# Kernel tuning notes

Measured on AMD Instinct MI355X. Metric: run time of the kernel, lower is better.

## Reference

```python
import jax, jax.numpy as jnp
import numpy as np

B, N, D = 32, 20, 64          # graph pairs, max node set size, node state dim
NODE_F, EDGE_F = 16, 8        # raw feature dims
E_PER, PROP = 40, 5           # edges per graph, propagation steps
NC2 = N * (N - 1) // 2        # 190
TEMP, ITERS = 0.1, 20         # sinkhorn temperature / iterations
SRC, DST = np.triu_indices(N, 1)   # source_list / destination_list (len NC2)


def _lin(k, fin, fout):
    return jax.random.normal(k, (fin, fout), dtype=jnp.float32) / np.sqrt(fin).astype(np.float32)


def setup_inputs():
    key = jax.random.key(0)
    ks = jax.random.split(key, 24)
    tn, te = 2 * B * N, 2 * B * E_PER
    gid = jnp.repeat(jnp.arange(2 * B), E_PER)   # edges stay within their graph
    inp = {
        'node_features': jax.random.normal(ks[0], (tn, NODE_F), jnp.float32),
        'edge_features': jax.random.normal(ks[1], (te, EDGE_F), jnp.float32),
        'query_adj': (jax.random.uniform(ks[2], (B, N, N)) < 0.3).astype(jnp.float32),
        'corpus_adj': (jax.random.uniform(ks[3], (B, N, N)) < 0.3).astype(jnp.float32),
        'from_idx': jax.random.randint(ks[4], (te,), 0, N) + gid * N,
        'to_idx': jax.random.randint(ks[5], (te,), 0, N) + gid * N,
    }
    # GraphEncoder
    inp['Wn'] = _lin(ks[6], NODE_F, D); inp['bn'] = jnp.zeros(D)
    inp['We'] = _lin(ks[7], EDGE_F, D); inp['be'] = jnp.zeros(D)
    # GraphPropLayer: message net (in 3D) and node-update net (in 2D)
    inp['Wm1'] = _lin(ks[8], 3 * D, D); inp['bm1'] = jnp.zeros(D)
    inp['Wm2'] = _lin(ks[9], D, D);     inp['bm2'] = jnp.zeros(D)
    inp['Wu1'] = _lin(ks[10], 2 * D, D); inp['bu1'] = jnp.zeros(D)
    inp['Wu2'] = _lin(ks[11], D, D);     inp['bu2'] = jnp.zeros(D)
    # node_sinkhorn_feature_layers: Linear(D,N) -> ReLU -> Linear(N,N)
    inp['Ws1'] = _lin(ks[12], D, N); inp['bs1'] = jnp.zeros(N)
    inp['Ws2'] = _lin(ks[13], N, N); inp['bs2'] = jnp.zeros(N)
    # lrl_network: Linear(2D+1, D) -> ReLU -> Linear(D, D)
    inp['Wl1'] = _lin(ks[14], 2 * D + 1, D); inp['bl1'] = jnp.zeros(D)
    inp['Wl2'] = _lin(ks[15], D, D);         inp['bl2'] = jnp.zeros(D)
    return inp


def _mlp2(x, W1, b1, W2, b2):
    return jax.nn.relu(x @ W1 + b1) @ W2 + b2


def _sinkhorn(log_alpha):
    la = log_alpha / TEMP
    for _ in range(ITERS):
        la = la - jax.nn.logsumexp(la, axis=2, keepdims=True)
        la = la - jax.nn.logsumexp(la, axis=1, keepdims=True)
    return jnp.exp(la)


def _nc2_edge_emb(H, adj, Wl1, bl1, Wl2, bl2):
    s, d = H[:, SRC], H[:, DST]          # [B, NC2, D]
    e = adj[:, SRC, DST][..., None]      # [B, NC2, 1]
    fwd = _mlp2(jnp.concatenate([s, d, e], -1), Wl1, bl1, Wl2, bl2)
    bwd = _mlp2(jnp.concatenate([d, s, e], -1), Wl1, bl1, Wl2, bl2)
    return fwd + bwd


def reference(node_features, edge_features, query_adj, corpus_adj, from_idx, to_idx,
              Wn, bn, We, be, Wm1, bm1, Wm2, bm2, Wu1, bu1, Wu2, bu2,
              Ws1, bs1, Ws2, bs2, Wl1, bl1, Wl2, bl2):
    # encoder
    h = node_features @ Wn + bn
    e = edge_features @ We + be
    # GMN-style gather -> MLP -> scatter propagation
    for _ in range(PROP):
        msg = _mlp2(jnp.concatenate([h[from_idx], h[to_idx], e], -1), Wm1, bm1, Wm2, bm2)
        agg = jax.ops.segment_sum(msg, to_idx, num_segments=2 * B * N)
        h = _mlp2(jnp.concatenate([h, agg], -1), Wu1, bu1, Wu2, bu2)
    # split_and_stack (all graphs have exactly N nodes): query even, corpus odd
    H = h.reshape(2 * B, N, D)
    Hq, Hc = H[0::2], H[1::2]
    # node Sinkhorn over L1 cdist of transformed features
    Tq = _mlp2(Hq, Ws1, bs1, Ws2, bs2)
    Tc = _mlp2(Hc, Ws1, bs1, Ws2, bs2)
    cost = jnp.abs(Tq[:, :, None, :] - Tc[:, None, :, :]).sum(-1)   # [B, N, N]
    P = _sinkhorn(-cost)                                            # node transport plan
    qe = _nc2_edge_emb(Hq, query_adj, Wl1, bl1, Wl2, bl2)           # [B, NC2, D]
    ce = _nc2_edge_emb(Hc, corpus_adj, Wl1, bl1, Wl2, bl2)
    # 4-way gather-multiply edge scores: [B, NC2, NC2]
    straight = P[:, SRC[:, None], SRC[None, :]] * P[:, DST[:, None], DST[None, :]]
    cross = P[:, SRC[:, None], DST[None, :]] * P[:, DST[:, None], SRC[None, :]]
    esi = jnp.maximum(straight, cross)                              # use_max=True
    eplan = _sinkhorn(jnp.log(esi + 1e-6))                          # use_second_sinkhorn_log
    # use_m_ms_edge=True: pairwise asymmetric L1 alignment distance
    diff = qe[:, :, None, :] - ce[:, None, :, :]                    # [B, NC2, NC2, D]
    dist = (eplan * (jax.nn.relu(diff).sum(-1) + jax.nn.relu(-diff).sum(-1))).sum((-1, -2))
    return dist                                                      # [B]
```

## Files before the change

kernel.cpp:

```cpp
#include <hip/hip_runtime.h>
#include <math.h>

#define B_     32
#define N_     20
#define D_     64
#define NODE_F 16
#define EDGE_F 8
#define E_PER  40
#define PROP   5
#define NC2    190
#define ITERS  20
#define INV_TEMP 10.0f
#define TN (2*B_*N_)
#define NG (2*B_)

struct PairTab { int s[NC2]; int d[NC2]; };
constexpr PairTab make_pairs() {
    PairTab t{};
    int idx = 0;
    for (int i = 0; i < N_; ++i)
        for (int j = i + 1; j < N_; ++j) { t.s[idx] = i; t.d[idx] = j; ++idx; }
    return t;
}
__device__ constexpr PairTab PAIRS = make_pairs();

__device__ __forceinline__ float rlane(float x, int k) {
    return __int_as_float(__builtin_amdgcn_readlane(__float_as_int(x), k));
}
template<int CTRL>
__device__ __forceinline__ float dppmov(float x) {
    return __int_as_float(__builtin_amdgcn_update_dpp(
        0, __float_as_int(x), CTRL, 0xf, 0xf, false));
}
__device__ __forceinline__ float rowsum16(float x) {
    x += dppmov<0x121>(x); x += dppmov<0x122>(x);
    x += dppmov<0x124>(x); x += dppmov<0x128>(x);
    return x;
}
__device__ __forceinline__ float rowmax16(float x) {
    x = fmaxf(x, dppmov<0x121>(x)); x = fmaxf(x, dppmov<0x122>(x));
    x = fmaxf(x, dppmov<0x124>(x)); x = fmaxf(x, dppmov<0x128>(x));
    return x;
}
__device__ __forceinline__ float nrcp(float x) {
    float r = __builtin_amdgcn_rcpf(x);
    r = r * fmaf(-x, r, 2.0f);
    return r;
}

__global__ __launch_bounds__(640) void k_prop(
    const float* __restrict__ nf, const float* __restrict__ ef,
    const int* __restrict__ fidx, const int* __restrict__ tidx,
    const float* __restrict__ Wn, const float* __restrict__ bn,
    const float* __restrict__ We, const float* __restrict__ be,
    const float* __restrict__ Wm1, const float* __restrict__ bm1,
    const float* __restrict__ Wm2, const float* __restrict__ bm2,
    const float* __restrict__ Wu1, const float* __restrict__ bu1,
    const float* __restrict__ Wu2, const float* __restrict__ bu2,
    float* __restrict__ hout)
{
    __shared__ float sh[20][64];
    __shared__ float se[40][64];
    __shared__ float sa[20][64];
    __shared__ short sF[40], sD[40];
    int g = blockIdx.x, t = threadIdx.x, w = t >> 6, l = t & 63;

    if (t < 40) {
        sF[t] = (short)(fidx[g * 40 + t] - g * 20);
        sD[t] = (short)(tidx[g * 40 + t] - g * 20);
    }
#pragma unroll
    for (int s = 0; s < 2; ++s) {
        int n = 2 * w + s;
        float a = bn[l];
#pragma unroll
        for (int k = 0; k < NODE_F; ++k) a += nf[(g * 20 + n) * NODE_F + k] * Wn[k * 64 + l];
        sh[n][l] = a; sa[n][l] = 0.f;
    }
#pragma unroll
    for (int s = 0; s < 4; ++s) {
        int e = 4 * w + s;
        float a = be[l];
#pragma unroll
        for (int k = 0; k < EDGE_F; ++k) a += ef[(g * 40 + e) * EDGE_F + k] * We[k * 64 + l];
        se[e][l] = a;
    }
    __syncthreads();

    for (int step = 0; step < PROP; ++step) {
        float xf[4], xt[4], xe[4]; int dst[4];
#pragma unroll
        for (int s = 0; s < 4; ++s) {
            int e = 4 * w + s;
            int fr = sF[e]; dst[s] = sD[e];
            xf[s] = sh[fr][l]; xt[s] = sh[dst[s]][l]; xe[s] = se[e][l];
        }
        float b1 = bm1[l];
        float acc[4];
#pragma unroll
        for (int s = 0; s < 4; ++s) acc[s] = b1;
#pragma unroll 4
        for (int k = 0; k < 64; ++k) {
            float w0 = Wm1[k * 64 + l];
            float w1 = Wm1[(64 + k) * 64 + l];
            float w2 = Wm1[(128 + k) * 64 + l];
#pragma unroll
            for (int s = 0; s < 4; ++s)
                acc[s] += rlane(xf[s], k) * w0 + rlane(xt[s], k) * w1 + rlane(xe[s], k) * w2;
        }
        float b2 = bm2[l];
        float out[4];
#pragma unroll
        for (int s = 0; s < 4; ++s) { acc[s] = fmaxf(acc[s], 0.f); out[s] = b2; }
#pragma unroll 4
        for (int k = 0; k < 64; ++k) {
            float ww = Wm2[k * 64 + l];
#pragma unroll
            for (int s = 0; s < 4; ++s) out[s] += rlane(acc[s], k) * ww;
        }
#pragma unroll
        for (int s = 0; s < 4; ++s) atomicAdd(&sa[dst[s]][l], out[s]);
        __syncthreads();

        float xh[2], xa[2];
#pragma unroll
        for (int s = 0; s < 2; ++s) {
            int n = 2 * w + s;
            xh[s] = sh[n][l]; xa[s] = sa[n][l];
        }
        float c1 = bu1[l];
        float a2[2];
#pragma unroll
        for (int s = 0; s < 2; ++s) a2[s] = c1;
#pragma unroll 4
        for (int k = 0; k < 64; ++k) {
            float wa = Wu1[k * 64 + l];
            float wb = Wu1[(64 + k) * 64 + l];
#pragma unroll
            for (int s = 0; s < 2; ++s)
                a2[s] += rlane(xh[s], k) * wa + rlane(xa[s], k) * wb;
        }
        float c2 = bu2[l];
        float o2[2];
#pragma unroll
        for (int s = 0; s < 2; ++s) { a2[s] = fmaxf(a2[s], 0.f); o2[s] = c2; }
#pragma unroll 4
        for (int k = 0; k < 64; ++k) {
            float ww = Wu2[k * 64 + l];
#pragma unroll
            for (int s = 0; s < 2; ++s) o2[s] += rlane(a2[s], k) * ww;
        }
#pragma unroll
        for (int s = 0; s < 2; ++s) {
            int n = 2 * w + s;
            sh[n][l] = o2[s]; sa[n][l] = 0.f;
        }
        __syncthreads();
    }
#pragma unroll
    for (int s = 0; s < 2; ++s) {
        int n = 2 * w + s;
        hout[(g * 20 + n) * 64 + l] = sh[n][l];
    }
}

__global__ __launch_bounds__(1024, 4) void k_fuse(
    const float* __restrict__ h,
    const float* __restrict__ qadj, const float* __restrict__ cadj,
    const float* __restrict__ Ws1, const float* __restrict__ bs1,
    const float* __restrict__ Ws2, const float* __restrict__ bs2,
    const float* __restrict__ Wl1, const float* __restrict__ bl1,
    const float* __restrict__ Wl2, const float* __restrict__ bl2,
    float* __restrict__ emb, float* __restrict__ eplan, float* __restrict__ dout)
{
    __shared__ short sQs[192], sQd[192];
    __shared__ float sP[N_][N_];
    __shared__ float sVbuf[192];
    __shared__ float region[12800];
    int t = threadIdx.x, w = t >> 6, l = t & 63;

    if (t < 192) {
        int tt = t < NC2 ? t : NC2 - 1;
        sQs[t] = (short)PAIRS.s[tt]; sQd[t] = (short)PAIRS.d[tt];
    }
    __syncthreads();

    if (blockIdx.x < 32) {
        int b = blockIdx.x;
        if (t == 0) dout[b] = 0.f;
        float* sT = region;
        float* sLa = region + 800;

        {
            int lk = (l < 20) ? l : 0;
#pragma unroll
            for (int s = 0; s < 3; ++s) {
                int r = w + 16 * s;
                if (r < 40) {
                    float hv = h[(b * 40 + r) * 64 + l];
                    float a = bs1[lk];
#pragma unroll 4
                    for (int ff = 0; ff < 64; ++ff) a += rlane(hv, ff) * Ws1[ff * 20 + lk];
                    a = fmaxf(a, 0.f);
                    float t2 = bs2[lk];
#pragma unroll
                    for (int j = 0; j < 20; ++j) t2 += rlane(a, j) * Ws2[j * 20 + lk];
                    if (l < 20) sT[(r >= 20) * 400 + (r % 20) * 20 + l] = t2;
                }
            }
        }
        __syncthreads();
        if (t < 400) {
            int i = t / 20, j = t % 20;
            float c = 0.f;
#pragma unroll
            for (int k = 0; k < 20; ++k) c += fabsf(sT[i * 20 + k] - sT[400 + j * 20 + k]);
            sLa[i * 20 + j] = -c * INV_TEMP;
        }
        __syncthreads();

        if (w == 0) {
            int q = l & 31, r2 = l >> 5;
            bool qok = (q < 20);
            float A20[10], u10[10];
#pragma unroll
            for (int i = 0; i < 10; ++i) {
                int r = 2 * i + r2;
                A20[i] = qok ? sLa[r * 20 + q] : -1e30f;
            }
            float vq = 0.f;
            for (int it = 0; it < ITERS; ++it) {
#pragma unroll
                for (int i = 0; i < 10; ++i) {
                    float x = A20[i] - vq;
                    float m = x;
#pragma unroll
                    for (int off = 16; off; off >>= 1) m = fmaxf(m, __shfl_xor(m, off));
                    float s = __expf(x - m);
#pragma unroll
                    for (int off = 16; off; off >>= 1) s += __shfl_xor(s, off);
                    u10[i] = m + __logf(s);
                }
                float pm = -1e30f;
#pragma unroll
                for (int i = 0; i < 10; ++i) pm = fmaxf(pm, A20[i] - u10[i]);
                float ps = 0.f;
#pragma unroll
                for (int i = 0; i < 10; ++i) ps += __expf(A20[i] - u10[i] - pm);
                float om = __shfl_xor(pm, 32), os = __shfl_xor(ps, 32);
                float M = fmaxf(pm, om);
                float S = ps * __expf(pm - M) + os * __expf(om - M);
                vq = M + __logf(S);
                if (!qok) vq = 0.f;
            }
#pragma unroll
            for (int i = 0; i < 10; ++i) {
                int r = 2 * i + r2;
                if (qok) sP[r][q] = __expf(A20[i] - u10[i] - vq);
            }
        }
        __syncthreads();

        int g4 = l >> 4, l16 = l & 15, rslot = w * 4 + g4;
        int sp[3], dp[3]; bool pv[3];
#pragma unroll
        for (int i = 0; i < 3; ++i) {
            int p = rslot + 64 * i;
            pv[i] = (p < NC2);
            int pc = pv[i] ? p : 0;
            sp[i] = sQs[pc]; dp[i] = sQd[pc];
        }
        int sq[12], dq[12]; bool qv[12];
#pragma unroll
        for (int j = 0; j < 12; ++j) {
            int q = l16 + 16 * j;
            qv[j] = (q < NC2);
            int qc = qv[j] ? q : 0;
            sq[j] = sQs[qc]; dq[j] = sQd[qc];
        }

        float AE[3][12];
#pragma unroll
        for (int i = 0; i < 3; ++i)
#pragma unroll
            for (int j = 0; j < 12; ++j) {
                if (pv[i] && qv[j]) {
                    float st = sP[sp[i]][sq[j]] * sP[dp[i]][dq[j]];
                    float cr = sP[sp[i]][dq[j]] * sP[dp[i]][sq[j]];
                    AE[i][j] = __logf(fmaxf(st, cr) + 1e-6f) * INV_TEMP;
                } else AE[i][j] = -1e30f;
            }

        float u[3];
#pragma unroll
        for (int i = 0; i < 3; ++i) {
            float m = -1e30f;
#pragma unroll
            for (int j = 0; j < 12; ++j) m = fmaxf(m, AE[i][j]);
            m = rowmax16(m);
            float s = 0.f;
#pragma unroll
            for (int j = 0; j < 12; ++j) s += __expf(AE[i][j] - m);
            s = rowsum16(s);
            u[i] = m + __logf(s);
            if (!pv[i]) u[i] = 0.f;
        }
#pragma unroll
        for (int j = 0; j < 12; ++j) {
            float pm = -1e30f;
#pragma unroll
            for (int i = 0; i < 3; ++i) if (pv[i]) pm = fmaxf(pm, AE[i][j] - u[i]);
            region[rslot * 200 + l16 + 16 * j] = pm;
        }
        __syncthreads();
        if (t < 192) {
            float M = -1e30f;
#pragma unroll
            for (int s = 0; s < 64; ++s) M = fmaxf(M, region[s * 200 + t]);
            sVbuf[t] = M;
        }
        __syncthreads();
        float Mj[12];
#pragma unroll
        for (int j = 0; j < 12; ++j) Mj[j] = sVbuf[l16 + 16 * j];
#pragma unroll
        for (int j = 0; j < 12; ++j) {
            float ps = 0.f;
#pragma unroll
            for (int i = 0; i < 3; ++i) if (pv[i]) ps += __expf(AE[i][j] - u[i] - Mj[j]);
            region[rslot * 200 + l16 + 16 * j] = ps;
        }
        __syncthreads();
        if (t < 192) {
            float S = 0.f;
#pragma unroll
            for (int s = 0; s < 64; ++s) S += region[s * 200 + t];
            sVbuf[t] = sVbuf[t] + __logf(fmaxf(S, 1e-37f));
        }
        __syncthreads();
#pragma unroll
        for (int j = 0; j < 12; ++j) Mj[j] = sVbuf[l16 + 16 * j];
#pragma unroll
        for (int i = 0; i < 3; ++i)
#pragma unroll
            for (int j = 0; j < 12; ++j) {
                float e = __expf(AE[i][j] - u[i] - Mj[j]);
                AE[i][j] = (pv[i] && qv[j]) ? e : 0.f;
            }
        __syncthreads();

        float invS[3];
        for (int it = 0; it < ITERS - 1; ++it) {
#pragma unroll
            for (int i = 0; i < 3; ++i) {
                float s01 = AE[i][0] + AE[i][1], s23 = AE[i][2] + AE[i][3];
                float s45 = AE[i][4] + AE[i][5], s67 = AE[i][6] + AE[i][7];
                float s89 = AE[i][8] + AE[i][9], sab = AE[i][10] + AE[i][11];
                float S = ((s01 + s23) + (s45 + s67)) + (s89 + sab);
                S = rowsum16(S);
                invS[i] = nrcp(fmaxf(S, 1e-30f));
            }
#pragma unroll
            for (int j = 0; j < 12; ++j) {
                float pc = AE[0][j] * invS[0];
                pc = fmaf(AE[1][j], invS[1], pc);
                pc = fmaf(AE[2][j], invS[2], pc);
                region[rslot * 200 + l16 + 16 * j] = pc;
            }
            __syncthreads();
            if (t < 192) {
                float a0 = 0.f, a1 = 0.f, a2 = 0.f, a3 = 0.f;
#pragma unroll
                for (int s = 0; s < 16; ++s) {
                    a0 += region[(4 * s + 0) * 200 + t];
                    a1 += region[(4 * s + 1) * 200 + t];
                    a2 += region[(4 * s + 2) * 200 + t];
                    a3 += region[(4 * s + 3) * 200 + t];
                }
                float c = (a0 + a1) + (a2 + a3);
                sVbuf[t] = nrcp(fmaxf(c, 1e-30f));
            }
            __syncthreads();
            float ic[12];
#pragma unroll
            for (int j = 0; j < 12; ++j) ic[j] = sVbuf[l16 + 16 * j];
#pragma unroll
            for (int i = 0; i < 3; ++i)
#pragma unroll
                for (int j = 0; j < 12; ++j) {
                    float tmp = AE[i][j] * invS[i];
                    AE[i][j] = tmp * ic[j];
                }
        }

        float* ep = eplan + (size_t)b * NC2 * NC2;
#pragma unroll
        for (int i = 0; i < 3; ++i) {
            if (pv[i]) {
                int p = rslot + 64 * i;
                float* row = ep + (size_t)p * NC2;
#pragma unroll
                for (int j = 0; j < 12; ++j)
                    if (qv[j]) row[l16 + 16 * j] = AE[i][j];
            }
        }
    } else {
        int eb = blockIdx.x - 32, b = eb >> 2, qt = eb & 3;
        float b1 = bl1[l];
        float w128 = Wl1[128 * 64 + l];
        float b2 = 2.f * bl2[l];

        int base = qt * 96 + w * 6;
        float sv[6], dv[6], av[6]; bool val[6]; int gg[6], pp[6];
#pragma unroll
        for (int s = 0; s < 6; ++s) {
            int pl = base + s;
            val[s] = (pl < 380);
            int plc = val[s] ? pl : 0;
            gg[s] = (plc >= 190) ? 1 : 0;
            pp[s] = plc - gg[s] * 190;
            int sp = sQs[pp[s]], dp = sQd[pp[s]];
            sv[s] = h[(b * 40 + gg[s] * 20 + sp) * 64 + l];
            dv[s] = h[(b * 40 + gg[s] * 20 + dp) * 64 + l];
            const float* adj = gg[s] ? cadj : qadj;
            av[s] = adj[b * 400 + sp * 20 + dp];
        }
        float aF[6], aB[6];
#pragma unroll
        for (int s = 0; s < 6; ++s) { float t0 = b1 + av[s] * w128; aF[s] = t0; aB[s] = t0; }
#pragma unroll 2
        for (int k = 0; k < 64; ++k) {
            float w0 = Wl1[k * 64 + l];
            float w1 = Wl1[(64 + k) * 64 + l];
#pragma unroll
            for (int s = 0; s < 6; ++s) {
                float a = rlane(sv[s], k), c = rlane(dv[s], k);
                aF[s] += a * w0 + c * w1;
                aB[s] += c * w0 + a * w1;
            }
        }
        float hs[6], out[6];
#pragma unroll
        for (int s = 0; s < 6; ++s) { hs[s] = fmaxf(aF[s], 0.f) + fmaxf(aB[s], 0.f); out[s] = b2; }
#pragma unroll 4
        for (int k = 0; k < 64; ++k) {
            float ww = Wl2[k * 64 + l];
#pragma unroll
            for (int s = 0; s < 6; ++s) out[s] += rlane(hs[s], k) * ww;
        }
#pragma unroll
        for (int s = 0; s < 6; ++s)
            if (val[s]) emb[((size_t)(2 * b + gg[s]) * NC2 + pp[s]) * 64 + l] = out[s];
    }
}

__global__ __launch_bounds__(256) void k_dist(
    const float* __restrict__ emb, const float* __restrict__ eplan, float* __restrict__ dout)
{
    int b = blockIdx.x, c = blockIdx.y;
    int w = threadIdx.x >> 6, l = threadIdx.x & 63;
    const float* qe = emb + (size_t)(2 * b) * NC2 * D_;
    const float* ce = emb + (size_t)(2 * b + 1) * NC2 * D_;
    const float* W = eplan + (size_t)b * NC2 * NC2;
    float acc = 0.f;
    int pbase = c * 16 + w * 4;
    for (int i = 0; i < 4; ++i) {
        int p = pbase + i;
        if (p >= NC2) break;
        float qv = qe[(size_t)p * D_ + l];
        const float* wrow = W + (size_t)p * NC2;
        for (int q = 0; q < NC2; ++q)
            acc += wrow[q] * fabsf(qv - ce[(size_t)q * D_ + l]);
    }
#pragma unroll
    for (int off = 32; off; off >>= 1) acc += __shfl_xor(acc, off);
    if (l == 0) atomicAdd(&dout[b], acc);
}

extern "C" void kernel_launch(void* const* d_in, const int* in_sizes, int n_in,
                              void* d_out, int out_size, void* d_ws, size_t ws_size,
                              hipStream_t stream)
{
    const float* nf   = (const float*)d_in[0];
    const float* ef   = (const float*)d_in[1];
    const float* qadj = (const float*)d_in[2];
    const float* cadj = (const float*)d_in[3];
    const int*   fidx = (const int*)d_in[4];
    const int*   tidx = (const int*)d_in[5];
    const float* Wn  = (const float*)d_in[6];  const float* bn  = (const float*)d_in[7];
    const float* We  = (const float*)d_in[8];  const float* be  = (const float*)d_in[9];
    const float* Wm1 = (const float*)d_in[10]; const float* bm1 = (const float*)d_in[11];
    const float* Wm2 = (const float*)d_in[12]; const float* bm2 = (const float*)d_in[13];
    const float* Wu1 = (const float*)d_in[14]; const float* bu1 = (const float*)d_in[15];
    const float* Wu2 = (const float*)d_in[16]; const float* bu2 = (const float*)d_in[17];
    const float* Ws1 = (const float*)d_in[18]; const float* bs1 = (const float*)d_in[19];
    const float* Ws2 = (const float*)d_in[20]; const float* bs2 = (const float*)d_in[21];
    const float* Wl1 = (const float*)d_in[22]; const float* bl1 = (const float*)d_in[23];
    const float* Wl2 = (const float*)d_in[24]; const float* bl2 = (const float*)d_in[25];

    float* ws    = (float*)d_ws;
    float* h     = ws;
    float* emb   = h + (size_t)TN * 64;
    float* eplan = emb + (size_t)NG * NC2 * 64;
    float* dout  = (float*)d_out;

    k_prop<<<NG, 640, 0, stream>>>(nf, ef, fidx, tidx, Wn, bn, We, be,
                                   Wm1, bm1, Wm2, bm2, Wu1, bu1, Wu2, bu2, h);
    k_fuse<<<160, 1024, 0, stream>>>(h, qadj, cadj, Ws1, bs1, Ws2, bs2,
                                     Wl1, bl1, Wl2, bl2, emb, eplan, dout);
    k_dist<<<dim3(B_, 12), 256, 0, stream>>>(emb, eplan, dout);
}
```

Before: 375.6 us.

## Factor message MLP per node, stage weights in LDS, shuffle-reduce sinkhorn partials

k_prop now splits the first message-layer matmul by linearity. It computes the from and to projections once per node (20 rows instead of 40 edges x 2) and precomputes the edge projection once before the propagation loop. All propagation weights are staged into LDS, and the kernel moves to 1024 threads per block. In k_fuse, the edge-sinkhorn column partials are pre-reduced with cross-lane shuffles so the LDS reduction reads 16 slots instead of 64, and the lrl weights are staged into LDS. In exchange, k_prop adds many extra barriers and repeated weight copies each step.

```diff
diff --git a/kernel.cpp b/kernel.cpp
--- a/kernel.cpp
+++ b/kernel.cpp
@@ -48,7 +48,7 @@
     return r;
 }
 
-__global__ __launch_bounds__(640) void k_prop(
+__global__ __launch_bounds__(1024, 4) void k_prop(
     const float* __restrict__ nf, const float* __restrict__ ef,
     const int* __restrict__ fidx, const int* __restrict__ tidx,
     const float* __restrict__ Wn, const float* __restrict__ bn,
@@ -59,8 +59,10 @@
     const float* __restrict__ Wu2, const float* __restrict__ bu2,
     float* __restrict__ hout)
 {
+    __shared__ __align__(16) float wbuf[8192];
     __shared__ float sh[20][64];
-    __shared__ float se[40][64];
+    __shared__ float sE1[40][64];
+    __shared__ float sFT[40][64];
     __shared__ float sa[20][64];
     __shared__ short sF[40], sD[40];
     int g = blockIdx.x, t = threadIdx.x, w = t >> 6, l = t & 63;
@@ -69,99 +71,105 @@
         sF[t] = (short)(fidx[g * 40 + t] - g * 20);
         sD[t] = (short)(tidx[g * 40 + t] - g * 20);
     }
-#pragma unroll
-    for (int s = 0; s < 2; ++s) {
-        int n = 2 * w + s;
+    for (int n = w; n < 20; n += 16) {
         float a = bn[l];
 #pragma unroll
         for (int k = 0; k < NODE_F; ++k) a += nf[(g * 20 + n) * NODE_F + k] * Wn[k * 64 + l];
         sh[n][l] = a; sa[n][l] = 0.f;
     }
-#pragma unroll
-    for (int s = 0; s < 4; ++s) {
-        int e = 4 * w + s;
-        float a = be[l];
-#pragma unroll
-        for (int k = 0; k < EDGE_F; ++k) a += ef[(g * 40 + e) * EDGE_F + k] * We[k * 64 + l];
-        se[e][l] = a;
+    {
+        const float4* s4 = (const float4*)(Wm1 + 128 * 64);
+        float4* d4 = (float4*)wbuf;
+        for (int i = t; i < 1024; i += 1024) d4[i] = s4[i];
     }
     __syncthreads();
+    for (int e = w; e < 40; e += 16) {
+        float em = be[l];
+#pragma unroll
+        for (int k = 0; k < EDGE_F; ++k) em += ef[(g * 40 + e) * EDGE_F + k] * We[k * 64 + l];
+        float a = bm1[l];
+#pragma unroll 4
+        for (int k = 0; k < 64; ++k) a += rlane(em, k) * wbuf[k * 64 + l];
+        sE1[e][l] = a;
+    }
 
     for (int step = 0; step < PROP; ++step) {
-        float xf[4], xt[4], xe[4]; int dst[4];
-#pragma unroll
-        for (int s = 0; s < 4; ++s) {
-            int e = 4 * w + s;
-            int fr = sF[e]; dst[s] = sD[e];
-            xf[s] = sh[fr][l]; xt[s] = sh[dst[s]][l]; xe[s] = se[e][l];
-        }
-        float b1 = bm1[l];
-        float acc[4];
-#pragma unroll
-        for (int s = 0; s < 4; ++s) acc[s] = b1;
-#pragma unroll 4
-        for (int k = 0; k < 64; ++k) {
-            float w0 = Wm1[k * 64 + l];
-            float w1 = Wm1[(64 + k) * 64 + l];
-            float w2 = Wm1[(128 + k) * 64 + l];
-#pragma unroll
-            for (int s = 0; s < 4; ++s)
-                acc[s] += rlane(xf[s], k) * w0 + rlane(xt[s], k) * w1 + rlane(xe[s], k) * w2;
-        }
-        float b2 = bm2[l];
-        float out[4];
-#pragma unroll
-        for (int s = 0; s < 4; ++s) { acc[s] = fmaxf(acc[s], 0.f); out[s] = b2; }
-#pragma unroll 4
-        for (int k = 0; k < 64; ++k) {
-            float ww = Wm2[k * 64 + l];
-#pragma unroll
-            for (int s = 0; s < 4; ++s) out[s] += rlane(acc[s], k) * ww;
-        }
-#pragma unroll
-        for (int s = 0; s < 4; ++s) atomicAdd(&sa[dst[s]][l], out[s]);
-        __syncthreads();
-
-        float xh[2], xa[2];
-#pragma unroll
-        for (int s = 0; s < 2; ++s) {
-            int n = 2 * w + s;
-            xh[s] = sh[n][l]; xa[s] = sa[n][l];
-        }
-        float c1 = bu1[l];
+        __syncthreads();
+        {
+            const float4* s4 = (const float4*)Wm1;
+            float4* d4 = (float4*)wbuf;
+            for (int i = t; i < 2048; i += 1024) d4[i] = s4[i];
+        }
+        __syncthreads();
+        {
+            int part = w >> 3;
+            int wl = w & 7;
+            for (int n = wl; n < 20; n += 8) {
+                float xh = sh[n][l];
+                float a = 0.f;
+#pragma unroll 4
+                for (int k = 0; k < 64; ++k)
+                    a += rlane(xh, k) * wbuf[(part * 64 + k) * 64 + l];
+                sFT[part * 20 + n][l] = a;
+            }
+        }
+        __syncthreads();
+        {
+            const float4* s4 = (const float4*)Wm2;
+            float4* d4 = (float4*)wbuf;
+            for (int i = t; i < 1024; i += 1024) d4[i] = s4[i];
+        }
+        __syncthreads();
+        for (int e = w; e < 40; e += 16) {
+            int fr = sF[e], to = sD[e];
+            float a1 = fmaxf(sFT[fr][l] + sFT[20 + to][l] + sE1[e][l], 0.f);
+            float o = bm2[l];
+#pragma unroll 4
+            for (int k = 0; k < 64; ++k) o += rlane(a1, k) * wbuf[k * 64 + l];
+            atomicAdd(&sa[to][l], o);
+        }
+        __syncthreads();
+        {
+            const float4* s4 = (const float4*)Wu1;
+            float4* d4 = (float4*)wbuf;
+            for (int i = t; i < 2048; i += 1024) d4[i] = s4[i];
+        }
+        __syncthreads();
         float a2[2];
 #pragma unroll
-        for (int s = 0; s < 2; ++s) a2[s] = c1;
-#pragma unroll 4
-        for (int k = 0; k < 64; ++k) {
-            float wa = Wu1[k * 64 + l];
-            float wb = Wu1[(64 + k) * 64 + l];
-#pragma unroll
-            for (int s = 0; s < 2; ++s)
-                a2[s] += rlane(xh[s], k) * wa + rlane(xa[s], k) * wb;
-        }
-        float c2 = bu2[l];
-        float o2[2];
-#pragma unroll
-        for (int s = 0; s < 2; ++s) { a2[s] = fmaxf(a2[s], 0.f); o2[s] = c2; }
-#pragma unroll 4
-        for (int k = 0; k < 64; ++k) {
-            float ww = Wu2[k * 64 + l];
-#pragma unroll
-            for (int s = 0; s < 2; ++s) o2[s] += rlane(a2[s], k) * ww;
-        }
-#pragma unroll
-        for (int s = 0; s < 2; ++s) {
-            int n = 2 * w + s;
-            sh[n][l] = o2[s]; sa[n][l] = 0.f;
-        }
-        __syncthreads();
-    }
-#pragma unroll
-    for (int s = 0; s < 2; ++s) {
-        int n = 2 * w + s;
-        hout[(g * 20 + n) * 64 + l] = sh[n][l];
-    }
+        for (int ii = 0; ii < 2; ++ii) {
+            int n = w + 16 * ii;
+            if (n < 20) {
+                float xh = sh[n][l], xa = sa[n][l];
+                float a = bu1[l];
+#pragma unroll 4
+                for (int k = 0; k < 64; ++k) {
+                    a += rlane(xh, k) * wbuf[k * 64 + l];
+                    a += rlane(xa, k) * wbuf[(64 + k) * 64 + l];
+                }
+                a2[ii] = fmaxf(a, 0.f);
+            } else a2[ii] = 0.f;
+        }
+        __syncthreads();
+        {
+            const float4* s4 = (const float4*)Wu2;
+            float4* d4 = (float4*)wbuf;
+            for (int i = t; i < 1024; i += 1024) d4[i] = s4[i];
+        }
+        __syncthreads();
+#pragma unroll
+        for (int ii = 0; ii < 2; ++ii) {
+            int n = w + 16 * ii;
+            if (n < 20) {
+                float o = bu2[l];
+#pragma unroll 4
+                for (int k = 0; k < 64; ++k) o += rlane(a2[ii], k) * wbuf[k * 64 + l];
+                sh[n][l] = o; sa[n][l] = 0.f;
+            }
+        }
+    }
+    __syncthreads();
+    for (int n = w; n < 20; n += 16) hout[(g * 20 + n) * 64 + l] = sh[n][l];
 }
 
 __global__ __launch_bounds__(1024, 4) void k_fuse(
@@ -176,7 +184,7 @@
     __shared__ short sQs[192], sQd[192];
     __shared__ float sP[N_][N_];
     __shared__ float sVbuf[192];
-    __shared__ float region[12800];
+    __shared__ __align__(16) float region[12800];
     int t = threadIdx.x, w = t >> 6, l = t & 63;
 
     if (t < 192) {
@@ -310,13 +318,15 @@
             float pm = -1e30f;
 #pragma unroll
             for (int i = 0; i < 3; ++i) if (pv[i]) pm = fmaxf(pm, AE[i][j] - u[i]);
-            region[rslot * 200 + l16 + 16 * j] = pm;
+            pm = fmaxf(pm, __shfl_xor(pm, 16));
+            pm = fmaxf(pm, __shfl_xor(pm, 32));
+            if (g4 == 0) region[w * 200 + l16 + 16 * j] = pm;
         }
         __syncthreads();
         if (t < 192) {
             float M = -1e30f;
 #pragma unroll
-            for (int s = 0; s < 64; ++s) M = fmaxf(M, region[s * 200 + t]);
+            for (int s = 0; s < 16; ++s) M = fmaxf(M, region[s * 200 + t]);
             sVbuf[t] = M;
         }
         __syncthreads();
@@ -328,13 +338,15 @@
             float ps = 0.f;
 #pragma unroll
             for (int i = 0; i < 3; ++i) if (pv[i]) ps += __expf(AE[i][j] - u[i] - Mj[j]);
-            region[rslot * 200 + l16 + 16 * j] = ps;
+            ps += __shfl_xor(ps, 16);
+            ps += __shfl_xor(ps, 32);
+            if (g4 == 0) region[w * 200 + l16 + 16 * j] = ps;
         }
         __syncthreads();
         if (t < 192) {
             float S = 0.f;
 #pragma unroll
-            for (int s = 0; s < 64; ++s) S += region[s * 200 + t];
+            for (int s = 0; s < 16; ++s) S += region[s * 200 + t];
             sVbuf[t] = sVbuf[t] + __logf(fmaxf(S, 1e-37f));
         }
         __syncthreads();
@@ -365,19 +377,15 @@
                 float pc = AE[0][j] * invS[0];
                 pc = fmaf(AE[1][j], invS[1], pc);
                 pc = fmaf(AE[2][j], invS[2], pc);
-                region[rslot * 200 + l16 + 16 * j] = pc;
+                pc += __shfl_xor(pc, 16);
+                pc += __shfl_xor(pc, 32);
+                if (g4 == 0) region[w * 200 + l16 + 16 * j] = pc;
             }
             __syncthreads();
             if (t < 192) {
-                float a0 = 0.f, a1 = 0.f, a2 = 0.f, a3 = 0.f;
-#pragma unroll
-                for (int s = 0; s < 16; ++s) {
-                    a0 += region[(4 * s + 0) * 200 + t];
-                    a1 += region[(4 * s + 1) * 200 + t];
-                    a2 += region[(4 * s + 2) * 200 + t];
-                    a3 += region[(4 * s + 3) * 200 + t];
-                }
-                float c = (a0 + a1) + (a2 + a3);
+                float c = 0.f;
+#pragma unroll
+                for (int s = 0; s < 16; ++s) c += region[s * 200 + t];
                 sVbuf[t] = nrcp(fmaxf(c, 1e-30f));
             }
             __syncthreads();
@@ -406,9 +414,20 @@
         }
     } else {
         int eb = blockIdx.x - 32, b = eb >> 2, qt = eb & 3;
+        float* wb1 = region;
+        float* wb2 = region + 8192;
+        {
+            const float4* s1 = (const float4*)Wl1;
+            float4* d1 = (float4*)wb1;
+            for (int i = t; i < 2048; i += 1024) d1[i] = s1[i];
+            const float4* s2 = (const float4*)Wl2;
+            float4* d2 = (float4*)wb2;
+            if (t < 1024) d2[t] = s2[t];
+        }
         float b1 = bl1[l];
         float w128 = Wl1[128 * 64 + l];
         float b2 = 2.f * bl2[l];
+        __syncthreads();
 
         int base = qt * 96 + w * 6;
         float sv[6], dv[6], av[6]; bool val[6]; int gg[6], pp[6];
@@ -430,8 +449,8 @@
         for (int s = 0; s < 6; ++s) { float t0 = b1 + av[s] * w128; aF[s] = t0; aB[s] = t0; }
 #pragma unroll 2
         for (int k = 0; k < 64; ++k) {
-            float w0 = Wl1[k * 64 + l];
-            float w1 = Wl1[(64 + k) * 64 + l];
+            float w0 = wb1[k * 64 + l];
+            float w1 = wb1[(64 + k) * 64 + l];
 #pragma unroll
             for (int s = 0; s < 6; ++s) {
                 float a = rlane(sv[s], k), c = rlane(dv[s], k);
@@ -444,7 +463,7 @@
         for (int s = 0; s < 6; ++s) { hs[s] = fmaxf(aF[s], 0.f) + fmaxf(aB[s], 0.f); out[s] = b2; }
 #pragma unroll 4
         for (int k = 0; k < 64; ++k) {
-            float ww = Wl2[k * 64 + l];
+            float ww = wb2[k * 64 + l];
 #pragma unroll
             for (int s = 0; s < 6; ++s) out[s] += rlane(hs[s], k) * ww;
         }
@@ -504,8 +523,8 @@
     float* eplan = emb + (size_t)NG * NC2 * 64;
     float* dout  = (float*)d_out;
 
-    k_prop<<<NG, 640, 0, stream>>>(nf, ef, fidx, tidx, Wn, bn, We, be,
-                                   Wm1, bm1, Wm2, bm2, Wu1, bu1, Wu2, bu2, h);
+    k_prop<<<NG, 1024, 0, stream>>>(nf, ef, fidx, tidx, Wn, bn, We, be,
+                                    Wm1, bm1, Wm2, bm2, Wu1, bu1, Wu2, bu2, h);
     k_fuse<<<160, 1024, 0, stream>>>(h, qadj, cadj, Ws1, bs1, Ws2, bs2,
                                      Wl1, bl1, Wl2, bl2, emb, eplan, dout);
     k_dist<<<dim3(B_, 12), 256, 0, stream>>>(emb, eplan, dout);
```

Result: faster. 350.9 us (-6.6%).
